# Optimization experiments

Measured on AMD Instinct MI355X. Metric: run time of the kernel, lower is better.

Reference implementation:

```python
import jax, jax.numpy as jnp
import numpy as np

HQ, HKV, D = 16, 2, 128   # num_heads_q, num_heads_kv, head_dim
G = HQ // HKV             # q heads per kv head (repeat_interleave factor)


def setup_inputs() -> dict:
    key = jax.random.key(0)
    ks = jax.random.split(key, 6)
    B, T, C = 2, 2048, 2048
    def w(k, shape):
        return jax.random.normal(k, shape, jnp.float32) * (1.0 / np.sqrt(shape[0]).astype(np.float32))
    x = jax.random.normal(ks[0], (B, T, C), jnp.float32)
    Wq = w(ks[1], (C, HQ * D))
    Wk = w(ks[2], (C, HKV * D))
    Wv = w(ks[3], (C, HKV * D))
    Wo = w(ks[4], (HQ * D, C))
    Wg = w(ks[5], (C, HQ))
    # causal mask: True where attention is disallowed (j > i)
    mask = jnp.triu(jnp.ones((T, T), dtype=bool), k=1)[None, None]  # (1,1,T,T)
    return {"x": x, "mask": mask, "Wq": Wq, "Wk": Wk, "Wv": Wv, "Wo": Wo, "Wg": Wg}


def reference(x, mask, Wq, Wk, Wv, Wo, Wg):
    B, T, C = x.shape
    # repeat_interleave(G, dim=heads) means q head h uses kv head h // G,
    # so group q heads as (HKV, G) instead of materializing repeated K/V.
    q = (x @ Wq).reshape(B, T, HKV, G, D).transpose(0, 2, 3, 1, 4)  # (B,HKV,G,T,D)
    k = (x @ Wk).reshape(B, T, HKV, D).transpose(0, 2, 1, 3)        # (B,HKV,T,D)
    v = (x @ Wv).reshape(B, T, HKV, D).transpose(0, 2, 1, 3)        # (B,HKV,T,D)
    scale = jnp.float32(1.0 / np.sqrt(D))
    scores = jnp.einsum('bkgtd,bksd->bkgts', q, k) * scale          # (B,HKV,G,T,T)
    scores = jnp.where(mask[:, None], jnp.float32(-1e9), scores)    # causal fill
    attn = jax.nn.softmax(scores, axis=-1)
    # post-softmax sigmoid gate, one scalar per (batch, q-head, query token)
    gates = jax.nn.sigmoid(x @ Wg)                                   # (B,T,HQ)
    gates = gates.transpose(0, 2, 1).reshape(B, HKV, G, T)           # (B,HKV,G,T)
    out = jnp.einsum('bkgts,bksd->btkgd', attn * gates[..., None], v)
    out = out.reshape(B, T, HQ * D)
    return out @ Wo
```

## Files before the change

kernel.cpp:

```cpp
#include <hip/hip_runtime.h>
#include <hip/hip_bf16.h>
#include <math.h>

#define HQ 16
#define HKV 2
#define D 128
#define B_SZ 2
#define T_SZ 2048
#define C_SZ 2048
#define QKVN 2688

#define C_Q 0.12753102f
#define C_G 1.44269504f

typedef __attribute__((ext_vector_type(8))) short short8;
typedef __attribute__((ext_vector_type(4))) float floatx4;

static __device__ __forceinline__ float fexp2(float x) {
    return __builtin_amdgcn_exp2f(x);
}

static __device__ __forceinline__ unsigned short f2b(float f) {
    union { float f; unsigned u; } x; x.f = f;
    return (unsigned short)((x.u + 0x7fffu + ((x.u >> 16) & 1u)) >> 16);
}

static __device__ __forceinline__ unsigned int pk2(float a, float b) {
    float2 t; t.x = a; t.y = b;
    __hip_bfloat162 h = __float22bfloat162_rn(t);
    return *(unsigned int*)&h;
}

static __device__ __forceinline__ void load_lds16(const void* g, void* l) {
    __builtin_amdgcn_global_load_lds(
        (const __attribute__((address_space(1))) void*)g,
        (__attribute__((address_space(3))) void*)l,
        16, 0, 0);
}

static __device__ __forceinline__ void tr32(
    const float* __restrict__ in, unsigned short* __restrict__ out,
    int R, int Cc, float premul, int bx, int by, float (*t)[33])
{
    const int bc = bx * 32, br = by * 32;
    const int tid = threadIdx.x;
    const int r = tid >> 3, c4 = (tid & 7) * 4;
    float4 v = *(const float4*)(in + (size_t)(br + r) * Cc + bc + c4);
    t[r][c4 + 0] = v.x; t[r][c4 + 1] = v.y; t[r][c4 + 2] = v.z; t[r][c4 + 3] = v.w;
    __syncthreads();
    ushort4 o;
    o.x = f2b(t[c4 + 0][r] * premul); o.y = f2b(t[c4 + 1][r] * premul);
    o.z = f2b(t[c4 + 2][r] * premul); o.w = f2b(t[c4 + 3][r] * premul);
    *(ushort4*)(out + (size_t)(bc + r) * R + br + c4) = o;
}

__global__ __launch_bounds__(256) void prep_kernel(
    const float* __restrict__ x,  const float* __restrict__ Wq,
    const float* __restrict__ Wk, const float* __restrict__ Wv,
    const float* __restrict__ Wo, const float* __restrict__ Wg,
    unsigned short* __restrict__ xb, unsigned short* __restrict__ Wqkvt,
    unsigned short* __restrict__ Wot)
{
    __shared__ float t[32][33];
    const int bid = blockIdx.x;
    const int tid = threadIdx.x;
    if (bid < 4096) {
        int i = bid * 2048 + tid * 8;
        float4 a = *(const float4*)(x + i);
        float4 b = *(const float4*)(x + i + 4);
        ushort4 o0, o1;
        o0.x = f2b(a.x); o0.y = f2b(a.y); o0.z = f2b(a.z); o0.w = f2b(a.w);
        o1.x = f2b(b.x); o1.y = f2b(b.y); o1.z = f2b(b.z); o1.w = f2b(b.w);
        *(ushort4*)(xb + i) = o0;
        *(ushort4*)(xb + i + 4) = o1;
    } else if (bid < 8192) {
        int n = bid - 4096;
        tr32(Wq, Wqkvt, C_SZ, HQ * D, C_Q, n & 63, n >> 6, t);
    } else if (bid < 8704) {
        int n = bid - 8192;
        tr32(Wk, Wqkvt + (size_t)(HQ * D) * C_SZ, C_SZ, HKV * D, 1.0f, n & 7, n >> 3, t);
    } else if (bid < 9216) {
        int n = bid - 8704;
        tr32(Wv, Wqkvt + (size_t)(HQ * D + HKV * D) * C_SZ, C_SZ, HKV * D, 1.0f, n & 7, n >> 3, t);
    } else if (bid < 13312) {
        int n = bid - 9216;
        tr32(Wo, Wot, HQ * D, C_SZ, 1.0f, n & 63, n >> 6, t);
    } else {
        int k = (bid - 13312) * 256 + tid;
        const float4* wr = (const float4*)(Wg + (size_t)k * 16);
        float4 w0 = wr[0], w1 = wr[1], w2 = wr[2], w3 = wr[3];
        float w[16] = {w0.x, w0.y, w0.z, w0.w, w1.x, w1.y, w1.z, w1.w,
                       w2.x, w2.y, w2.z, w2.w, w3.x, w3.y, w3.z, w3.w};
        unsigned short* out = Wqkvt + (size_t)(HQ * D + 2 * HKV * D) * C_SZ;
        #pragma unroll
        for (int h = 0; h < 16; ++h)
            out[(size_t)h * C_SZ + k] = f2b(w[h] * C_G);
    }
}

__global__ __launch_bounds__(256) void gemm_bt_bf16(
    const unsigned short* __restrict__ A, const unsigned short* __restrict__ Bt,
    float* __restrict__ Cf, unsigned short* __restrict__ Cb,
    unsigned short* __restrict__ Vt, int M, int N, int K, int out_bf16)
{
    __shared__ __align__(16) unsigned short SM[8448];
    unsigned short* As = SM;
    unsigned short* Bs = SM + 4096;
    const int tid = threadIdx.x;
    const int lane = tid & 63, wave = tid >> 6;
    const int l15 = lane & 15, quad = lane >> 4;
    const int wr = wave >> 1, wc = wave & 1;
    const int bm = blockIdx.y * 128, bn = blockIdx.x * 128;

    floatx4 zero = {0.f, 0.f, 0.f, 0.f};
    floatx4 acc[4][4];
    #pragma unroll
    for (int i = 0; i < 4; ++i)
        #pragma unroll
        for (int j = 0; j < 4; ++j) acc[i][j] = zero;

    int arow[2], acol[2];
    #pragma unroll
    for (int it = 0; it < 2; ++it) {
        int idx = it * 256 + tid;
        int row = idx >> 2, sb = idx & 3;
        int cb = sb ^ ((row >> 1) & 3);
        arow[it] = row; acol[it] = cb * 8;
    }
    const int sw = quad ^ ((l15 >> 1) & 3);

    for (int k0 = 0; k0 < K; k0 += 32) {
        __syncthreads();
        #pragma unroll
        for (int it = 0; it < 2; ++it) {
            load_lds16(A  + (size_t)(bm + arow[it]) * K + k0 + acol[it],
                       &As[(it * 256 + wave * 64) * 8]);
            load_lds16(Bt + (size_t)(bn + arow[it]) * K + k0 + acol[it],
                       &Bs[(it * 256 + wave * 64) * 8]);
        }
        __syncthreads();

        short8 af[4], bf[4];
        #pragma unroll
        for (int mt = 0; mt < 4; ++mt)
            af[mt] = *(const short8*)&As[((wr * 64 + mt * 16 + l15) * 4 + sw) * 8];
        #pragma unroll
        for (int nt = 0; nt < 4; ++nt)
            bf[nt] = *(const short8*)&Bs[((wc * 64 + nt * 16 + l15) * 4 + sw) * 8];
        #pragma unroll
        for (int mt = 0; mt < 4; ++mt)
            #pragma unroll
            for (int nt = 0; nt < 4; ++nt)
                acc[mt][nt] = __builtin_amdgcn_mfma_f32_16x16x32_bf16(
                    af[mt], bf[nt], acc[mt][nt], 0, 0, 0);
    }

    if (Vt && (bn == 2304 || bn == 2432)) {
        unsigned short (*Ct)[132] = (unsigned short(*)[132])SM;
        const int bb = bm >> 11;
        const int tl = bm & 2047;
        #pragma unroll
        for (int vn = 0; vn < 2; ++vn) {
            __syncthreads();
            if (wc == vn) {
                #pragma unroll
                for (int mt = 0; mt < 4; ++mt)
                    #pragma unroll
                    for (int nt = 0; nt < 4; ++nt)
                        #pragma unroll
                        for (int r = 0; r < 4; ++r)
                            Ct[nt * 16 + l15][wr * 64 + mt * 16 + quad * 4 + r] =
                                f2b(acc[mt][nt][r]);
            }
            __syncthreads();
            int row = tid >> 2, cs = (tid & 3) * 32;
            int vrow = (bn - 2304) + vn * 64 + row;
            unsigned short* dst = Vt + ((size_t)bb * (HKV * D) + vrow) * T_SZ + tl + cs;
            const unsigned short* src = &Ct[row][cs];
            short8 v0 = *(const short8*)(src + 0);
            short8 v1 = *(const short8*)(src + 8);
            short8 v2 = *(const short8*)(src + 16);
            short8 v3 = *(const short8*)(src + 24);
            *(short8*)(dst + 0)  = v0; *(short8*)(dst + 8)  = v1;
            *(short8*)(dst + 16) = v2; *(short8*)(dst + 24) = v3;
        }
        return;
    }

    #pragma unroll
    for (int mt = 0; mt < 4; ++mt)
        #pragma unroll
        for (int nt = 0; nt < 4; ++nt)
            #pragma unroll
            for (int r = 0; r < 4; ++r) {
                int m = bm + wr * 64 + mt * 16 + quad * 4 + r;
                int n = bn + wc * 64 + nt * 16 + l15;
                if (out_bf16) Cb[(size_t)m * N + n] = f2b(acc[mt][nt][r]);
                else          Cf[(size_t)m * N + n] = acc[mt][nt][r];
            }
}

__global__ __launch_bounds__(256) void attn_mfma(
    const unsigned short* __restrict__ QKV, const unsigned short* __restrict__ Vt,
    unsigned short* __restrict__ Ob)
{
    __shared__ __align__(16) unsigned short SMEM[64 * 128 + 128 * 64 + 4 * 16 * 72];
    unsigned short* Ks = SMEM;
    unsigned short* Vs = SMEM + 64 * 128;
    unsigned short* Ps = SMEM + 64 * 128 + 128 * 64;
    unsigned short* Lo = SMEM;

    const int bh = blockIdx.x;
    const int qt = (int)gridDim.y - 1 - (int)blockIdx.y;
    const int b = bh >> 4, h = bh & 15, kvh = h >> 3;
    const int tid = threadIdx.x;
    const int lane = tid & 63, w = tid >> 6;
    const int l15 = lane & 15, quad = lane >> 4;
    const int q_local = w * 16 + l15;
    const float BIAS = 32.0f;

    short8 aq[4];
    {
        const unsigned short* qp = QKV + (size_t)(b * T_SZ + qt * 64 + q_local) * QKVN
                                       + h * D + quad * 8;
        #pragma unroll
        for (int kd = 0; kd < 4; ++kd) aq[kd] = *(const short8*)(qp + kd * 32);
    }

    const unsigned short* kg[4];
    const unsigned short* vg[4];
    #pragma unroll
    for (int it = 0; it < 4; ++it) {
        int Bi = it * 256 + tid;
        int kr = Bi >> 4, kc = ((Bi & 15) ^ (kr & 15)) * 8;
        kg[it] = QKV + (size_t)(b * T_SZ + kr) * QKVN + HQ * D + kvh * D + kc;
        int vr = Bi >> 3, vc = ((Bi & 7) ^ (vr & 7)) * 8;
        vg[it] = Vt + (size_t)((b * HKV + kvh) * D + vr) * T_SZ + vc;
    }

    floatx4 zero = {0.f, 0.f, 0.f, 0.f};
    floatx4 oacc[8];
    #pragma unroll
    for (int dt = 0; dt < 8; ++dt) oacc[dt] = zero;
    float l_part = 0.f;

    for (int kt = 0; kt <= qt; ++kt) {
        __syncthreads();
        #pragma unroll
        for (int it = 0; it < 4; ++it) {
            load_lds16(kg[it] + (size_t)kt * 64 * QKVN, &Ks[(it * 256 + w * 64) * 8]);
            load_lds16(vg[it] + kt * 64,                &Vs[(it * 256 + w * 64) * 8]);
        }
        __syncthreads();

        floatx4 sacc[4];
        #pragma unroll
        for (int nt = 0; nt < 4; ++nt) sacc[nt] = zero;
        #pragma unroll
        for (int kd = 0; kd < 4; ++kd)
            #pragma unroll
            for (int nt = 0; nt < 4; ++nt) {
                short8 ak = *(const short8*)&Ks[((nt * 16 + l15) * 16 + ((kd * 4 + quad) ^ l15)) * 8];
                sacc[nt] = __builtin_amdgcn_mfma_f32_16x16x32_bf16(ak, aq[kd], sacc[nt], 0, 0, 0);
            }

        float p[4][4];
        if (kt == qt) {
            #pragma unroll
            for (int nt = 0; nt < 4; ++nt)
                #pragma unroll
                for (int r = 0; r < 4; ++r) {
                    float e = fexp2(sacc[nt][r] - BIAS);
                    p[nt][r] = (nt * 16 + quad * 4 + r > q_local) ? 0.f : e;
                }
        } else {
            #pragma unroll
            for (int nt = 0; nt < 4; ++nt)
                #pragma unroll
                for (int r = 0; r < 4; ++r)
                    p[nt][r] = fexp2(sacc[nt][r] - BIAS);
        }
        #pragma unroll
        for (int nt = 0; nt < 4; ++nt) {
            l_part += (p[nt][0] + p[nt][1]) + (p[nt][2] + p[nt][3]);
            uint2 pw;
            pw.x = pk2(p[nt][0], p[nt][1]);
            pw.y = pk2(p[nt][2], p[nt][3]);
            *(uint2*)&Ps[(w * 16 + l15) * 72 + nt * 16 + quad * 4] = pw;
        }

        #pragma unroll
        for (int kk = 0; kk < 2; ++kk) {
            short8 bp = *(const short8*)&Ps[(w * 16 + l15) * 72 + kk * 32 + quad * 8];
            #pragma unroll
            for (int dt = 0; dt < 8; ++dt) {
                short8 av = *(const short8*)&Vs[((dt * 16 + l15) * 8 + ((kk * 4 + quad) ^ (l15 & 7))) * 8];
                oacc[dt] = __builtin_amdgcn_mfma_f32_16x16x32_bf16(av, bp, oacc[dt], 0, 0, 0);
            }
        }
    }

    float l = l_part;
    l += __shfl_xor(l, 16);
    l += __shfl_xor(l, 32);

    __syncthreads();
    {
        int token = b * T_SZ + qt * 64 + q_local;
        unsigned short gl = QKV[(size_t)token * QKVN + HQ * D + HKV * D * 2 + h];
        union { unsigned u; float f; } gx; gx.u = ((unsigned)gl) << 16;
        float g = 1.0f / (1.0f + fexp2(-gx.f));
        float f = g / l;
        #pragma unroll
        for (int dt = 0; dt < 8; ++dt) {
            uint2 ov;
            ov.x = pk2(oacc[dt][0] * f, oacc[dt][1] * f);
            ov.y = pk2(oacc[dt][2] * f, oacc[dt][3] * f);
            *(uint2*)&Lo[(size_t)q_local * 136 + dt * 16 + quad * 4] = ov;
        }
    }
    __syncthreads();
    {
        int row = tid >> 2, c0 = (tid & 3) * 32;
        size_t tok = (size_t)(b * T_SZ + qt * 64 + row);
        unsigned short* op = Ob + tok * (HQ * D) + h * D + c0;
        const unsigned short* lp = &Lo[(size_t)row * 136 + c0];
        short8 v0 = *(const short8*)(lp + 0);
        short8 v1 = *(const short8*)(lp + 8);
        short8 v2 = *(const short8*)(lp + 16);
        short8 v3 = *(const short8*)(lp + 24);
        *(short8*)(op + 0)  = v0; *(short8*)(op + 8)  = v1;
        *(short8*)(op + 16) = v2; *(short8*)(op + 24) = v3;
    }
}

extern "C" void kernel_launch(void* const* d_in, const int* in_sizes, int n_in,
                              void* d_out, int out_size, void* d_ws, size_t ws_size,
                              hipStream_t stream) {
    const float* x  = (const float*)d_in[0];
    const float* Wq = (const float*)d_in[2];
    const float* Wk = (const float*)d_in[3];
    const float* Wv = (const float*)d_in[4];
    const float* Wo = (const float*)d_in[5];
    const float* Wg = (const float*)d_in[6];
    float* out = (float*)d_out;

    const size_t KB = 1ull << 10;
    char* p = (char*)d_ws;
    unsigned short* xb    = (unsigned short*)(p);
    unsigned short* Ob    = xb;
    unsigned short* Wqkvt = (unsigned short*)(p + 16384 * KB);
    unsigned short* Wot   = (unsigned short*)(p + 27136 * KB);
    unsigned short* QKV   = (unsigned short*)(p + 35328 * KB);
    unsigned short* Vt    = (unsigned short*)(p + 56832 * KB);
    const int BT = B_SZ * T_SZ;

    prep_kernel<<<dim3(13320), 256, 0, stream>>>(x, Wq, Wk, Wv, Wo, Wg, xb, Wqkvt, Wot);

    gemm_bt_bf16<<<dim3(QKVN / 128, BT / 128), 256, 0, stream>>>(
        xb, Wqkvt, nullptr, QKV, Vt, BT, QKVN, C_SZ, 1);

    attn_mfma<<<dim3(B_SZ * HQ, T_SZ / 64), 256, 0, stream>>>(QKV, Vt, Ob);

    gemm_bt_bf16<<<dim3(C_SZ / 128, BT / 128), 256, 0, stream>>>(
        Ob, Wot, out, nullptr, nullptr, BT, C_SZ, HQ * D, 0);
}
```

Baseline: 310.6 us.

## Replace GEMM with double-buffered 256-wide tile kernel and separate V transpose

Replaces the 128x128 single-buffered bf16 GEMM with a templated 512-thread kernel using 256-wide N tiles and K=64 stages. It double-buffers LDS and register fragments and raises wave priority during MFMA, so global loads overlap with matrix math. The fused V-transpose epilogue moves into a separate small vtrans kernel. The larger tiles cut global traffic per FLOP, but the kernel now uses a large LDS footprint, which limits occupancy, and reads padding rows past N.

```diff
diff --git a/kernel.cpp b/kernel.cpp
--- a/kernel.cpp
+++ b/kernel.cpp
@@ -98,106 +98,143 @@
     }
 }
 
-__global__ __launch_bounds__(256) void gemm_bt_bf16(
+template<int BM>
+__global__ __launch_bounds__(512, 2) void gemm256(
     const unsigned short* __restrict__ A, const unsigned short* __restrict__ Bt,
     float* __restrict__ Cf, unsigned short* __restrict__ Cb,
-    unsigned short* __restrict__ Vt, int M, int N, int K, int out_bf16)
+    int Nreal, int K, int out_bf16)
 {
-    __shared__ __align__(16) unsigned short SM[8448];
-    unsigned short* As = SM;
-    unsigned short* Bs = SM + 4096;
+    constexpr int MT = BM / 32;
+    constexpr int LA = BM / 64;
+    constexpr int VM = LA + 4;
+    __shared__ __align__(16) unsigned short SM[2][(BM + 256) * 64];
+
     const int tid = threadIdx.x;
     const int lane = tid & 63, wave = tid >> 6;
     const int l15 = lane & 15, quad = lane >> 4;
-    const int wr = wave >> 1, wc = wave & 1;
-    const int bm = blockIdx.y * 128, bn = blockIdx.x * 128;
+    const int wm = wave >> 2, wn = wave & 3;
+    const int bm0 = blockIdx.y * BM, bn0 = blockIdx.x * 256;
+    const int NT = K >> 6;
+
+    unsigned aoff[LA], boff[4];
+    #pragma unroll
+    for (int j = 0; j < LA; ++j) {
+        int c = j * 512 + tid, r = c >> 3, sb = c & 7;
+        aoff[j] = (unsigned)(((bm0 + r) * K + ((sb ^ (r & 7)) << 3)) * 2);
+    }
+    #pragma unroll
+    for (int j = 0; j < 4; ++j) {
+        int c = j * 512 + tid, r = c >> 3, sb = c & 7;
+        boff[j] = (unsigned)(((bn0 + r) * K + ((sb ^ (r & 7)) << 3)) * 2);
+    }
 
     floatx4 zero = {0.f, 0.f, 0.f, 0.f};
-    floatx4 acc[4][4];
-    #pragma unroll
-    for (int i = 0; i < 4; ++i)
+    floatx4 acc[MT][4];
+    #pragma unroll
+    for (int i = 0; i < MT; ++i)
         #pragma unroll
         for (int j = 0; j < 4; ++j) acc[i][j] = zero;
 
-    int arow[2], acol[2];
-    #pragma unroll
-    for (int it = 0; it < 2; ++it) {
-        int idx = it * 256 + tid;
-        int row = idx >> 2, sb = idx & 3;
-        int cb = sb ^ ((row >> 1) & 3);
-        arow[it] = row; acol[it] = cb * 8;
-    }
-    const int sw = quad ^ ((l15 >> 1) & 3);
-
-    for (int k0 = 0; k0 < K; k0 += 32) {
-        __syncthreads();
-        #pragma unroll
-        for (int it = 0; it < 2; ++it) {
-            load_lds16(A  + (size_t)(bm + arow[it]) * K + k0 + acol[it],
-                       &As[(it * 256 + wave * 64) * 8]);
-            load_lds16(Bt + (size_t)(bn + arow[it]) * K + k0 + acol[it],
-                       &Bs[(it * 256 + wave * 64) * 8]);
-        }
-        __syncthreads();
-
-        short8 af[4], bf[4];
-        #pragma unroll
-        for (int mt = 0; mt < 4; ++mt)
-            af[mt] = *(const short8*)&As[((wr * 64 + mt * 16 + l15) * 4 + sw) * 8];
+    auto STAGE = [&](int b, int t) {
+        #pragma unroll
+        for (int j = 0; j < LA; ++j)
+            load_lds16((const char*)A + aoff[j] + (size_t)t * 128,
+                       &SM[b][(j * 512 + wave * 64) * 8]);
+        #pragma unroll
+        for (int j = 0; j < 4; ++j)
+            load_lds16((const char*)Bt + boff[j] + (size_t)t * 128,
+                       &SM[b][BM * 64 + (j * 512 + wave * 64) * 8]);
+    };
+
+    auto RD = [&](short8 (&FA)[MT], short8 (&FB)[4], int b, int kk) {
+        const unsigned short* Sa = &SM[b][0];
+        const unsigned short* Sb = &SM[b][BM * 64];
+        const int swz = ((kk << 2) + quad) ^ (l15 & 7);
+        #pragma unroll
+        for (int mt = 0; mt < MT; ++mt)
+            FA[mt] = *(const short8*)&Sa[(wm * (BM / 2) + mt * 16 + l15) * 64 + swz * 8];
         #pragma unroll
         for (int nt = 0; nt < 4; ++nt)
-            bf[nt] = *(const short8*)&Bs[((wc * 64 + nt * 16 + l15) * 4 + sw) * 8];
-        #pragma unroll
-        for (int mt = 0; mt < 4; ++mt)
+            FB[nt] = *(const short8*)&Sb[(wn * 64 + nt * 16 + l15) * 64 + swz * 8];
+    };
+
+    auto MM = [&](short8 (&FA)[MT], short8 (&FB)[4]) {
+        __builtin_amdgcn_s_setprio(1);
+        #pragma unroll
+        for (int mt = 0; mt < MT; ++mt)
             #pragma unroll
             for (int nt = 0; nt < 4; ++nt)
                 acc[mt][nt] = __builtin_amdgcn_mfma_f32_16x16x32_bf16(
-                    af[mt], bf[nt], acc[mt][nt], 0, 0, 0);
-    }
-
-    if (Vt && (bn == 2304 || bn == 2432)) {
-        unsigned short (*Ct)[132] = (unsigned short(*)[132])SM;
-        const int bb = bm >> 11;
-        const int tl = bm & 2047;
-        #pragma unroll
-        for (int vn = 0; vn < 2; ++vn) {
-            __syncthreads();
-            if (wc == vn) {
+                    FA[mt], FB[nt], acc[mt][nt], 0, 0, 0);
+        __builtin_amdgcn_s_setprio(0);
+    };
+
+    short8 RaA[MT], RaB[4], RbA[MT], RbB[4];
+
+    STAGE(0, 0);
+    STAGE(1, 1);
+    asm volatile("s_waitcnt vmcnt(%0)" :: "n"(VM) : "memory");
+    __builtin_amdgcn_sched_barrier(0);
+    __builtin_amdgcn_s_barrier();
+    __builtin_amdgcn_sched_barrier(0);
+    RD(RaA, RaB, 0, 0);
+
+    #pragma unroll 2
+    for (int t = 0; t < NT; ++t) {
+        const int b = t & 1;
+        RD(RbA, RbB, b, 1);
+        MM(RaA, RaB);
+        asm volatile("s_waitcnt lgkmcnt(0)" ::: "memory");
+        __builtin_amdgcn_sched_barrier(0);
+        __builtin_amdgcn_s_barrier();
+        __builtin_amdgcn_sched_barrier(0);
+        if (t + 2 < NT) {
+            STAGE(b, t + 2);
+            asm volatile("s_waitcnt vmcnt(%0)" :: "n"(VM) : "memory");
+        } else if (t + 1 < NT) {
+            asm volatile("s_waitcnt vmcnt(0)" ::: "memory");
+        }
+        __builtin_amdgcn_sched_barrier(0);
+        __builtin_amdgcn_s_barrier();
+        __builtin_amdgcn_sched_barrier(0);
+        if (t + 1 < NT) RD(RaA, RaB, b ^ 1, 0);
+        MM(RbA, RbB);
+    }
+
+    #pragma unroll
+    for (int mt = 0; mt < MT; ++mt)
+        #pragma unroll
+        for (int nt = 0; nt < 4; ++nt) {
+            const int n = bn0 + wn * 64 + nt * 16 + l15;
+            if (n < Nreal) {
                 #pragma unroll
-                for (int mt = 0; mt < 4; ++mt)
-                    #pragma unroll
-                    for (int nt = 0; nt < 4; ++nt)
-                        #pragma unroll
-                        for (int r = 0; r < 4; ++r)
-                            Ct[nt * 16 + l15][wr * 64 + mt * 16 + quad * 4 + r] =
-                                f2b(acc[mt][nt][r]);
+                for (int r = 0; r < 4; ++r) {
+                    const int m = bm0 + wm * (BM / 2) + mt * 16 + quad * 4 + r;
+                    if (out_bf16) Cb[(size_t)m * Nreal + n] = f2b(acc[mt][nt][r]);
+                    else          Cf[(size_t)m * Nreal + n] = acc[mt][nt][r];
+                }
             }
-            __syncthreads();
-            int row = tid >> 2, cs = (tid & 3) * 32;
-            int vrow = (bn - 2304) + vn * 64 + row;
-            unsigned short* dst = Vt + ((size_t)bb * (HKV * D) + vrow) * T_SZ + tl + cs;
-            const unsigned short* src = &Ct[row][cs];
-            short8 v0 = *(const short8*)(src + 0);
-            short8 v1 = *(const short8*)(src + 8);
-            short8 v2 = *(const short8*)(src + 16);
-            short8 v3 = *(const short8*)(src + 24);
-            *(short8*)(dst + 0)  = v0; *(short8*)(dst + 8)  = v1;
-            *(short8*)(dst + 16) = v2; *(short8*)(dst + 24) = v3;
-        }
-        return;
-    }
-
-    #pragma unroll
-    for (int mt = 0; mt < 4; ++mt)
-        #pragma unroll
-        for (int nt = 0; nt < 4; ++nt)
-            #pragma unroll
-            for (int r = 0; r < 4; ++r) {
-                int m = bm + wr * 64 + mt * 16 + quad * 4 + r;
-                int n = bn + wc * 64 + nt * 16 + l15;
-                if (out_bf16) Cb[(size_t)m * N + n] = f2b(acc[mt][nt][r]);
-                else          Cf[(size_t)m * N + n] = acc[mt][nt][r];
-            }
+        }
+}
+
+__global__ __launch_bounds__(256) void vtrans(
+    const unsigned short* __restrict__ QKV, unsigned short* __restrict__ Vt)
+{
+    __shared__ unsigned short T[64][72];
+    const int tid = threadIdx.x;
+    const int tok0 = blockIdx.x * 64, vd0 = blockIdx.y * 64;
+    const int r = tid >> 2, c = (tid & 3) * 16;
+    const unsigned short* src = QKV + (size_t)(tok0 + r) * QKVN
+                                    + (HQ * D + HKV * D) + vd0 + c;
+    short8 v0 = *(const short8*)src;
+    short8 v1 = *(const short8*)(src + 8);
+    #pragma unroll
+    for (int j = 0; j < 8; ++j) { T[c + j][r] = v0[j]; T[c + 8 + j][r] = v1[j]; }
+    __syncthreads();
+    const int b = tok0 >> 11, tl = tok0 & 2047;
+    unsigned short* dst = Vt + ((size_t)b * (HKV * D) + vd0 + r) * T_SZ + tl + c;
+    *(short8*)dst       = *(const short8*)&T[r][c];
+    *(short8*)(dst + 8) = *(const short8*)&T[r][c + 8];
 }
 
 __global__ __launch_bounds__(256) void attn_mfma(
@@ -357,11 +394,13 @@
 
     prep_kernel<<<dim3(13320), 256, 0, stream>>>(x, Wq, Wk, Wv, Wo, Wg, xb, Wqkvt, Wot);
 
-    gemm_bt_bf16<<<dim3(QKVN / 128, BT / 128), 256, 0, stream>>>(
-        xb, Wqkvt, nullptr, QKV, Vt, BT, QKVN, C_SZ, 1);
+    gemm256<256><<<dim3(11, BT / 256), 512, 0, stream>>>(
+        xb, Wqkvt, nullptr, QKV, QKVN, C_SZ, 1);
+
+    vtrans<<<dim3(BT / 64, (HKV * D) / 64), 256, 0, stream>>>(QKV, Vt);
 
     attn_mfma<<<dim3(B_SZ * HQ, T_SZ / 64), 256, 0, stream>>>(QKV, Vt, Ob);
 
-    gemm_bt_bf16<<<dim3(C_SZ / 128, BT / 128), 256, 0, stream>>>(
-        Ob, Wot, out, nullptr, nullptr, BT, C_SZ, HQ * D, 0);
-}
+    gemm256<128><<<dim3(C_SZ / 256, BT / 128), 512, 0, stream>>>(
+        Ob, Wot, out, nullptr, C_SZ, HQ * D, 0);
+}
```

New measurement: 287.2 us. 7.5% less time.
